# Kernel optimization log

Hardware: AMD Instinct MI355X
Metric: run time of the kernel (lower is better)

## Reference

```python
import jax, jax.numpy as jnp
import numpy as np
from jax import lax

BETA = 0.5
IPOT_ITERS = 20


def cosine_cost(x, y):
    # x: [bs, n, D], y: [bs, m, D] -> 1 - cos_sim, [bs, n, m]
    x = x / (jnp.linalg.norm(x, axis=2, keepdims=True) + 1e-12)
    y = y / (jnp.linalg.norm(y, axis=2, keepdims=True) + 1e-12)
    return 1.0 - jnp.einsum('bnd,bmd->bnm', x, y)


def ipot_T(C, miu, nu, beta=BETA, iters=IPOT_ITERS):
    bs, n, m = C.shape
    A = jnp.exp(-C / beta)                    # [bs, n, m]
    sigma0 = jnp.ones((bs, m, 1), C.dtype) / m
    T0 = jnp.ones((bs, n, m), C.dtype)

    def step(carry, _):
        T, sigma = carry
        T = A * T
        delta = miu[:, :, None] / (T @ sigma + 1e-6)            # [bs, n, 1]
        sigma = nu[:, :, None] / (jnp.swapaxes(T, 1, 2) @ delta + 1e-6)  # [bs, m, 1]
        T = delta * T * jnp.swapaxes(sigma, 1, 2)
        return (T, sigma), None

    (T, _), _ = lax.scan(step, (T0, sigma0), None, length=iters)
    return lax.stop_gradient(T)  # original code detaches T


def ipot_distance(C):
    bs, n, m = C.shape
    miu = jnp.ones((bs, n), C.dtype) / n
    nu = jnp.ones((bs, m), C.dtype) / m
    T = ipot_T(C, miu, nu)
    return -jnp.sum(T * C, axis=(1, 2))  # note: original (un-exponentiated) C


def setup_inputs() -> dict:
    key = jax.random.key(0)
    k1, k2, k3, k4 = jax.random.split(key, 4)
    bs, n_sp, n_tm, D = 128, 196, 32, 768
    return {
        'spatial1': jax.random.normal(k1, (bs, n_sp, D), dtype=jnp.float32),
        'spatial2': jax.random.normal(k2, (bs, n_sp, D), dtype=jnp.float32),
        'temporal1': jax.random.normal(k3, (bs, n_tm, D), dtype=jnp.float32),
        'temporal2': jax.random.normal(k4, (bs, n_tm, D), dtype=jnp.float32),
    }


def reference(spatial1, spatial2, temporal1, temporal2):
    C_sp = cosine_cost(spatial1, spatial2)
    C_tm = cosine_cost(temporal1, temporal2)
    spatial_loss = ipot_distance(C_sp)
    temporal_loss = ipot_distance(C_tm)
    return spatial_loss.mean() + temporal_loss.mean()
```

## Files before the change

### kernel.cpp

```cpp
#include <hip/hip_runtime.h>
#include <hip/hip_bf16.h>
#include <cstdint>

typedef float f32x4 __attribute__((ext_vector_type(4)));
typedef __bf16 bf16x8 __attribute__((ext_vector_type(8)));

#define BS 128
#define NSP 196
#define NTM 32
#define DDIM 768

__device__ inline ushort4 f4_to_bf4(float4 v)
{
    ushort4 u;
    u.x = __builtin_bit_cast(unsigned short, (__bf16)v.x);
    u.y = __builtin_bit_cast(unsigned short, (__bf16)v.y);
    u.z = __builtin_bit_cast(unsigned short, (__bf16)v.z);
    u.w = __builtin_bit_cast(unsigned short, (__bf16)v.w);
    return u;
}

__device__ inline bf16x8 f4x2_to_bf8(float4 lo, float4 hi)
{
    bf16x8 r;
    r[0] = (__bf16)lo.x; r[1] = (__bf16)lo.y; r[2] = (__bf16)lo.z; r[3] = (__bf16)lo.w;
    r[4] = (__bf16)hi.x; r[5] = (__bf16)hi.y; r[6] = (__bf16)hi.z; r[7] = (__bf16)hi.w;
    return r;
}

__device__ inline float sumsq4(float4 a)
{
    return fmaf(a.x, a.x, fmaf(a.y, a.y, fmaf(a.z, a.z, a.w * a.w)));
}

__global__ __launch_bounds__(256)
void tm_norm_kernel(const float* __restrict__ tm1, const float* __restrict__ tm2,
                    float* __restrict__ inx_tm, float* __restrict__ iny_tm)
{
    int B = blockIdx.x;
    const float* src; float* inv;
    if (B < 1024) { src = tm1; inv = inx_tm; }
    else          { B -= 1024; src = tm2; inv = iny_tm; }
    const int row  = B * 4 + (threadIdx.x >> 6);
    const int lane = threadIdx.x & 63;
    const float4* p = reinterpret_cast<const float4*>(src + (size_t)row * DDIM);
    float ss = 0.f;
#pragma unroll
    for (int c = 0; c < 3; ++c) ss += sumsq4(p[lane + 64 * c]);
#pragma unroll
    for (int off = 32; off; off >>= 1) ss += __shfl_xor(ss, off, 64);
    if (lane == 0) inv[row] = 1.0f / (sqrtf(ss) + 1e-12f);
}

#define GA_LDS 18432
__global__ __launch_bounds__(448)
void cost_gemm_spf(const float* __restrict__ X, const float* __restrict__ Y,
                   __bf16* __restrict__ Aout)
{
    __shared__ __bf16 lds[2 * GA_LDS];
    float* ldsF = reinterpret_cast<float*>(lds);

    const int flat  = blockIdx.x;
    const int xcd   = flat & 7;
    const int s     = flat >> 3;
    const int b     = xcd * 16 + (s >> 2);
    const int ctile = s & 3;
    const int n0    = (ctile < 3) ? ctile * 64 : 132;

    const int tid  = threadIdx.x;
    const int w    = tid >> 6, lane = tid & 63;
    const int q    = lane >> 4, l16 = lane & 15;
    const int srow = tid >> 3;
    const int sslt = tid & 7;

    const float* Yb = Y + (size_t)b * NSP * DDIM;

    float4 aL[4], aH[4], bL, bH, b2L, b2H;
    float ssA[4] = {0.f, 0.f, 0.f, 0.f};
    float ssB = 0.f, ssB2 = 0.f;

    auto LOADS = [&](int k0) {
#pragma unroll
        for (int p = 0; p < 4; ++p) {
            int gr = b * NSP + srow + 56 * p;
            gr = min(gr, BS * NSP - 1);
            const float* sp = X + (size_t)gr * DDIM + k0 + sslt * 8;
            aL[p] = *reinterpret_cast<const float4*>(sp);
            aH[p] = *reinterpret_cast<const float4*>(sp + 4);
        }
        {
            const float* sp = Yb + (size_t)(n0 + srow) * DDIM + k0 + sslt * 8;
            bL = *reinterpret_cast<const float4*>(sp);
            bH = *reinterpret_cast<const float4*>(sp + 4);
        }
        if (tid < 64) {
            const float* sp = Yb + (size_t)(n0 + 56 + srow) * DDIM + k0 + sslt * 8;
            b2L = *reinterpret_cast<const float4*>(sp);
            b2H = *reinterpret_cast<const float4*>(sp + 4);
        }
    };
    auto WRITES = [&](int buf) {
#pragma unroll
        for (int p = 0; p < 4; ++p) {
            int r = srow + 56 * p;
            ssA[p] += sumsq4(aL[p]) + sumsq4(aH[p]);
            *reinterpret_cast<bf16x8*>(&lds[buf * GA_LDS + r * 64 + ((sslt ^ (r & 7)) << 3)]) =
                f4x2_to_bf8(aL[p], aH[p]);
        }
        {
            int r = srow;
            ssB += sumsq4(bL) + sumsq4(bH);
            *reinterpret_cast<bf16x8*>(&lds[buf * GA_LDS + 14336 + r * 64 + ((sslt ^ (r & 7)) << 3)]) =
                f4x2_to_bf8(bL, bH);
        }
        if (tid < 64) {
            int r = 56 + srow;
            ssB2 += sumsq4(b2L) + sumsq4(b2H);
            *reinterpret_cast<bf16x8*>(&lds[buf * GA_LDS + 14336 + r * 64 + ((sslt ^ (r & 7)) << 3)]) =
                f4x2_to_bf8(b2L, b2H);
        }
    };

    f32x4 acc[2][4];
#pragma unroll
    for (int i = 0; i < 2; ++i)
#pragma unroll
        for (int j = 0; j < 4; ++j) acc[i][j] = f32x4{0.f, 0.f, 0.f, 0.f};

    LOADS(0);
    int buf = 0;
    for (int kt = 0; kt < 12; ++kt) {
        WRITES(buf);
        if (kt < 11) LOADS((kt + 1) * 64);
        __syncthreads();
#pragma unroll
        for (int ks = 0; ks < 2; ++ks) {
            bf16x8 af[2], bf[4];
#pragma unroll
            for (int rt = 0; rt < 2; ++rt) {
                int r = w * 32 + rt * 16 + l16;
                af[rt] = *reinterpret_cast<const bf16x8*>(
                    &lds[buf * GA_LDS + r * 64 + (((ks * 4 + q) ^ (r & 7)) << 3)]);
            }
#pragma unroll
            for (int ct = 0; ct < 4; ++ct) {
                int r = ct * 16 + l16;
                bf[ct] = *reinterpret_cast<const bf16x8*>(
                    &lds[buf * GA_LDS + 14336 + r * 64 + (((ks * 4 + q) ^ (r & 7)) << 3)]);
            }
#pragma unroll
            for (int ct = 0; ct < 4; ++ct)
#pragma unroll
                for (int rt = 0; rt < 2; ++rt)
                    acc[rt][ct] = __builtin_amdgcn_mfma_f32_16x16x32_bf16(af[rt], bf[ct], acc[rt][ct], 0, 0, 0);
        }
        __syncthreads();
        buf ^= 1;
    }

#pragma unroll
    for (int p = 0; p < 4; ++p) ldsF[(srow + 56 * p) * 8 + sslt] = ssA[p];
    ldsF[1792 + srow * 8 + sslt] = ssB;
    if (tid < 64) ldsF[1792 + (56 + srow) * 8 + sslt] = ssB2;
    __syncthreads();

    float ivy[4];
#pragma unroll
    for (int ct = 0; ct < 4; ++ct) {
        int jr = ct * 16 + l16;
        f32x4 s0 = *reinterpret_cast<const f32x4*>(&ldsF[1792 + jr * 8]);
        f32x4 s1 = *reinterpret_cast<const f32x4*>(&ldsF[1792 + jr * 8 + 4]);
        float ss = (s0.x + s0.y) + (s0.z + s0.w) + (s1.x + s1.y) + (s1.z + s1.w);
        ivy[ct] = 1.0f / (sqrtf(ss) + 1e-12f);
    }
#pragma unroll
    for (int rt = 0; rt < 2; ++rt)
#pragma unroll
        for (int rr = 0; rr < 4; ++rr) {
            int i = w * 32 + rt * 16 + q * 4 + rr;
            if (i < NSP) {
                f32x4 s0 = *reinterpret_cast<const f32x4*>(&ldsF[i * 8]);
                f32x4 s1 = *reinterpret_cast<const f32x4*>(&ldsF[i * 8 + 4]);
                float ss = (s0.x + s0.y) + (s0.z + s0.w) + (s1.x + s1.y) + (s1.z + s1.w);
                float ivx = 1.0f / (sqrtf(ss) + 1e-12f);
#pragma unroll
                for (int ct = 0; ct < 4; ++ct) {
                    float cs = acc[rt][ct][rr] * ivx * ivy[ct];
                    Aout[(size_t)b * 65536 + (size_t)i * 256 + (n0 + ct * 16 + l16)] =
                        (__bf16)__expf(2.0f * cs - 2.0f);
                }
            }
        }
}

template<int WROWS, int NWAVES, int BN, int NPTS>
__global__ __launch_bounds__(NWAVES * 64)
void cost_gemm(const float* __restrict__ X, const float* __restrict__ Y,
               const float* __restrict__ invx, const float* __restrict__ invy,
               float* __restrict__ Aout)
{
    constexpr int MT = WROWS * NWAVES;
    constexpr int CT = BN / 16;
    constexpr int RT = WROWS / 16;
    constexpr int KP = 40;
    constexpr int NTH = NWAVES * 64;
    __shared__ __bf16 As[MT][KP];
    __shared__ __bf16 Bs[BN][KP];

    const int b    = blockIdx.y;
    const int row0 = blockIdx.x * MT;
    const int tid  = threadIdx.x;
    const int w    = tid >> 6, lane = tid & 63;
    const int q    = lane >> 4, l16 = lane & 15;
    const float* Xb = X + (size_t)b * NPTS * DDIM;
    const float* Yb = Y + (size_t)b * NPTS * DDIM;

    f32x4 acc[RT][CT];
#pragma unroll
    for (int i = 0; i < RT; ++i)
#pragma unroll
        for (int j = 0; j < CT; ++j) acc[i][j] = f32x4{0.f, 0.f, 0.f, 0.f};

    for (int k0 = 0; k0 < DDIM; k0 += 32) {
        __syncthreads();
        for (int idx = tid * 4; idx < MT * 32; idx += NTH * 4) {
            int r = idx >> 5, kk = idx & 31;
            int gr = row0 + r;
            float4 v = {0.f, 0.f, 0.f, 0.f};
            if (gr < NPTS) v = *reinterpret_cast<const float4*>(Xb + (size_t)gr * DDIM + k0 + kk);
            *reinterpret_cast<ushort4*>(&As[r][kk]) = f4_to_bf4(v);
        }
        for (int idx = tid * 4; idx < BN * 32; idx += NTH * 4) {
            int r = idx >> 5, kk = idx & 31;
            float4 v = {0.f, 0.f, 0.f, 0.f};
            if (r < NPTS) v = *reinterpret_cast<const float4*>(Yb + (size_t)r * DDIM + k0 + kk);
            *reinterpret_cast<ushort4*>(&Bs[r][kk]) = f4_to_bf4(v);
        }
        __syncthreads();

        bf16x8 af[RT];
#pragma unroll
        for (int rt = 0; rt < RT; ++rt)
            af[rt] = *reinterpret_cast<const bf16x8*>(&As[w * WROWS + rt * 16 + l16][q * 8]);
#pragma unroll
        for (int ct = 0; ct < CT; ++ct) {
            bf16x8 bfr = *reinterpret_cast<const bf16x8*>(&Bs[ct * 16 + l16][q * 8]);
#pragma unroll
            for (int rt = 0; rt < RT; ++rt)
                acc[rt][ct] = __builtin_amdgcn_mfma_f32_16x16x32_bf16(af[rt], bfr, acc[rt][ct], 0, 0, 0);
        }
    }

#pragma unroll
    for (int rt = 0; rt < RT; ++rt)
#pragma unroll
        for (int ct = 0; ct < CT; ++ct)
#pragma unroll
            for (int rr = 0; rr < 4; ++rr) {
                int i = row0 + w * WROWS + rt * 16 + q * 4 + rr;
                int j = ct * 16 + l16;
                if (i < NPTS && j < NPTS) {
                    float g  = acc[rt][ct][rr];
                    float cs = g * invx[b * NPTS + i] * invy[b * NPTS + j];
                    Aout[(size_t)b * NPTS * NPTS + (size_t)i * NPTS + j] = expf(-2.0f * (1.0f - cs));
                }
            }
}

__global__ __launch_bounds__(512, 1)
void ipot_lds(const __bf16* __restrict__ Asp, const float* __restrict__ Atm,
              float* __restrict__ out)
{
    __shared__ __bf16 Alds[224 * 256];
    __shared__ float  cpart[8 * 260];
    __shared__ float  svec[2][272];
    __shared__ float  wsum[8];

    const int B = blockIdx.x;
    if (B >= 128) {
        if (threadIdx.x >= 64) return;
        const int b = B - 128;
        const float* Ab = Atm + (size_t)b * NTM * NTM;
        const int lane = threadIdx.x;
        const int rh = lane >> 5, cj = lane & 31;
        constexpr float MIU = 1.f / NTM;
        float A[16], P[16];
#pragma unroll
        for (int k = 0; k < 16; ++k) {
            A[k] = Ab[(rh + 2 * k) * NTM + cj];
            P[k] = 1.f;
        }
        float sv = MIU;
        for (int it = 0; it < 20; ++it) {
#pragma unroll
            for (int k = 0; k < 16; ++k) {
                P[k] *= A[k];
                float acc = P[k] * sv;
                acc += __shfl_xor(acc, 1);
                acc += __shfl_xor(acc, 2);
                acc += __shfl_xor(acc, 4);
                acc += __shfl_xor(acc, 8);
                acc += __shfl_xor(acc, 16);
                P[k] *= MIU / (acc + 1e-6f);
            }
            float cssum = 0.f;
#pragma unroll
            for (int k = 0; k < 16; ++k) cssum += P[k];
            cssum += __shfl_xor(cssum, 32);
            float sg = MIU / (cssum + 1e-6f);
#pragma unroll
            for (int k = 0; k < 16; ++k) P[k] *= sg;
            sv = sg;
        }
        float acc = 0.f;
#pragma unroll
        for (int k = 0; k < 16; ++k)
            acc = fmaf(P[k], -0.5f * __logf(A[k]), acc);
#pragma unroll
        for (int off = 32; off; off >>= 1) acc += __shfl_xor(acc, off);
        if (lane == 0) atomicAdd(out, -acc * (1.f / BS));
        return;
    }

    const int b = (B & 7) * 16 + (B >> 3);
    const __bf16* Ab = Asp + (size_t)b * 65536;
    const int tid = threadIdx.x;
    const int w = tid >> 6, lane = tid & 63;
    const int rq = lane >> 4, cl = lane & 15;
    const int g = w * 4 + rq;
    const int colbase = cl * 8;
    constexpr float MIU = 1.f / NSP;

    for (int idx = tid; idx < NSP * 32; idx += 512) {
        int r = idx >> 5, c = idx & 31;
        bf16x8 v;
#pragma unroll
        for (int i = 0; i < 8; ++i) v[i] = (__bf16)0.f;
        if (c < 25) {
            v = *reinterpret_cast<const bf16x8*>(&Ab[(size_t)r * 256 + c * 8]);
            if (c == 24) { v[4] = (__bf16)0.f; v[5] = (__bf16)0.f; v[6] = (__bf16)0.f; v[7] = (__bf16)0.f; }
        }
        *reinterpret_cast<bf16x8*>(&Alds[r * 256 + c * 8]) = v;
    }
    {
        ushort4 z = {0, 0, 0, 0};
        for (int idx = tid; idx < 28 * 64; idx += 512) {
            int r = 196 + (idx >> 6), c4 = (idx & 63) << 2;
            *reinterpret_cast<ushort4*>(&Alds[r * 256 + c4]) = z;
        }
    }
    __syncthreads();

    float P[7][16];
#pragma unroll
    for (int k = 0; k < 7; ++k)
#pragma unroll
        for (int e = 0; e < 16; ++e) P[k][e] = 1.f;

    float sr[16];
#pragma unroll
    for (int e = 0; e < 16; ++e) {
        int j = (e < 8) ? (colbase + e) : (colbase + 128 + (e - 8));
        sr[e] = (j < NSP) ? MIU : 0.f;
    }

    for (int it = 0; it < 20; ++it) {
        float cs[16];
#pragma unroll
        for (int e = 0; e < 16; ++e) cs[e] = 0.f;

#pragma unroll
        for (int k = 0; k < 7; ++k) {
            const __bf16* ap = &Alds[(g + 32 * k) * 256 + colbase];
            bf16x8 a0 = *reinterpret_cast<const bf16x8*>(ap);
            bf16x8 a1 = *reinterpret_cast<const bf16x8*>(ap + 128);
            float racc = 0.f;
#pragma unroll
            for (int e = 0; e < 8; ++e) {
                P[k][e] *= (float)a0[e];
                racc = fmaf(P[k][e], sr[e], racc);
            }
#pragma unroll
            for (int e = 0; e < 8; ++e) {
                P[k][8 + e] *= (float)a1[e];
                racc = fmaf(P[k][8 + e], sr[8 + e], racc);
            }
            racc += __shfl_xor(racc, 1);
            racc += __shfl_xor(racc, 2);
            racc += __shfl_xor(racc, 4);
            racc += __shfl_xor(racc, 8);
            float delta = MIU / (racc + 1e-6f);
#pragma unroll
            for (int e = 0; e < 16; ++e) {
                P[k][e] *= delta;
                cs[e] += P[k][e];
            }
        }
#pragma unroll
        for (int e = 0; e < 16; ++e) {
            cs[e] += __shfl_xor(cs[e], 16);
            cs[e] += __shfl_xor(cs[e], 32);
        }
        if (rq == 0) {
            float* cp = &cpart[w * 260 + colbase];
            *reinterpret_cast<f32x4*>(cp)     = f32x4{cs[0], cs[1], cs[2], cs[3]};
            *reinterpret_cast<f32x4*>(cp + 4) = f32x4{cs[4], cs[5], cs[6], cs[7]};
            float* cp2 = cp + 128;
            *reinterpret_cast<f32x4*>(cp2)     = f32x4{cs[8], cs[9], cs[10], cs[11]};
            *reinterpret_cast<f32x4*>(cp2 + 4) = f32x4{cs[12], cs[13], cs[14], cs[15]};
        }
        __syncthreads();
        if (tid < 256) {
            float s0 = 0.f, s1 = 0.f;
#pragma unroll
            for (int gg = 0; gg < 8; gg += 2) {
                s0 += cpart[(gg + 0) * 260 + tid];
                s1 += cpart[(gg + 1) * 260 + tid];
            }
            float sum = s0 + s1;
            svec[it & 1][tid] = (tid < NSP) ? (MIU / (sum + 1e-6f)) : 0.f;
        }
        __syncthreads();
        {
            const float* sv = svec[it & 1];
            f32x4 t0 = *reinterpret_cast<const f32x4*>(&sv[colbase]);
            f32x4 t1 = *reinterpret_cast<const f32x4*>(&sv[colbase + 4]);
            f32x4 t2 = *reinterpret_cast<const f32x4*>(&sv[colbase + 128]);
            f32x4 t3 = *reinterpret_cast<const f32x4*>(&sv[colbase + 132]);
            sr[0] = t0.x; sr[1] = t0.y; sr[2] = t0.z; sr[3] = t0.w;
            sr[4] = t1.x; sr[5] = t1.y; sr[6] = t1.z; sr[7] = t1.w;
            sr[8] = t2.x; sr[9] = t2.y; sr[10] = t2.z; sr[11] = t2.w;
            sr[12] = t3.x; sr[13] = t3.y; sr[14] = t3.z; sr[15] = t3.w;
        }
#pragma unroll
        for (int k = 0; k < 7; ++k)
#pragma unroll
            for (int e = 0; e < 16; ++e) P[k][e] *= sr[e];
    }

    float acc = 0.f;
#pragma unroll
    for (int k = 0; k < 7; ++k) {
        const __bf16* ap = &Alds[(g + 32 * k) * 256 + colbase];
        bf16x8 a0 = *reinterpret_cast<const bf16x8*>(ap);
        bf16x8 a1 = *reinterpret_cast<const bf16x8*>(ap + 128);
#pragma unroll
        for (int e = 0; e < 8; ++e) {
            acc = fmaf(P[k][e],     -0.5f * __logf(fmaxf((float)a0[e], 1e-30f)), acc);
            acc = fmaf(P[k][8 + e], -0.5f * __logf(fmaxf((float)a1[e], 1e-30f)), acc);
        }
    }
#pragma unroll
    for (int off = 32; off; off >>= 1) acc += __shfl_xor(acc, off);
    if (lane == 0) wsum[w] = acc;
    __syncthreads();
    if (tid == 0) {
        float t = 0.f;
#pragma unroll
        for (int i = 0; i < 8; ++i) t += wsum[i];
        atomicAdd(out, -t * (1.f / BS));
    }
}

extern "C" void kernel_launch(void* const* d_in, const int* in_sizes, int n_in,
                              void* d_out, int out_size, void* d_ws, size_t ws_size,
                              hipStream_t stream)
{
    const float* sp1 = (const float*)d_in[0];
    const float* sp2 = (const float*)d_in[1];
    const float* tm1 = (const float*)d_in[2];
    const float* tm2 = (const float*)d_in[3];
    float* out = (float*)d_out;
    float* ws  = (float*)d_ws;

    float* inx_tm = ws;
    float* iny_tm = inx_tm + BS * NTM;
    float* A_tm   = iny_tm + BS * NTM;
    __bf16* A_sp  = (__bf16*)(ws + 139264);

    tm_norm_kernel<<<dim3(2048), 256, 0, stream>>>(tm1, tm2, inx_tm, iny_tm);

    cost_gemm_spf<<<dim3(512), 448, 0, stream>>>(sp1, sp2, A_sp);

    cost_gemm<16, 2, 32, NTM><<<dim3(1, BS), 128, 0, stream>>>(tm1, tm2, inx_tm, iny_tm, A_tm);

    (void)hipMemsetAsync(d_out, 0, sizeof(float), stream);

    ipot_lds<<<dim3(256), 512, 0, stream>>>(A_sp, A_tm, out);
}
```

Measured before the change: 177.6 us.

## Double IPOT block to 1024 threads and pad LDS row stride

The spatial IPOT kernel now runs 16 waves per batch instead of 8. Each thread holds 3-4 row groups of the transport plan instead of 7, and the column partial sums are reduced across 16 waves. The LDS row stride is padded from 256 to 264 to cut bank conflicts on row reads. The aim is more latency hiding and less per-thread serial work in the 20-iteration loop, at the cost of more register pressure per block, two barriers that now span more waves, and extra LDS use.

```diff
diff --git a/kernel.cpp b/kernel.cpp
--- a/kernel.cpp
+++ b/kernel.cpp
@@ -267,14 +267,15 @@
             }
 }
 
-__global__ __launch_bounds__(512, 1)
-void ipot_lds(const __bf16* __restrict__ Asp, const float* __restrict__ Atm,
-              float* __restrict__ out)
-{
-    __shared__ __bf16 Alds[224 * 256];
-    __shared__ float  cpart[8 * 260];
+#define ASTR 264
+__global__ __launch_bounds__(1024, 1)
+void ipot_all2(const __bf16* __restrict__ Asp, const float* __restrict__ Atm,
+               float* __restrict__ out)
+{
+    __shared__ __bf16 Alds[224 * ASTR];
+    __shared__ float  cpart[16 * 260];
     __shared__ float  svec[2][272];
-    __shared__ float  wsum[8];
+    __shared__ float  wsum[16];
 
     const int B = blockIdx.x;
     if (B >= 128) {
@@ -329,9 +330,10 @@
     const int rq = lane >> 4, cl = lane & 15;
     const int g = w * 4 + rq;
     const int colbase = cl * 8;
+    const bool w8 = (w < 8);
     constexpr float MIU = 1.f / NSP;
 
-    for (int idx = tid; idx < NSP * 32; idx += 512) {
+    for (int idx = tid; idx < NSP * 32; idx += 1024) {
         int r = idx >> 5, c = idx & 31;
         bf16x8 v;
 #pragma unroll
@@ -340,20 +342,22 @@
             v = *reinterpret_cast<const bf16x8*>(&Ab[(size_t)r * 256 + c * 8]);
             if (c == 24) { v[4] = (__bf16)0.f; v[5] = (__bf16)0.f; v[6] = (__bf16)0.f; v[7] = (__bf16)0.f; }
         }
-        *reinterpret_cast<bf16x8*>(&Alds[r * 256 + c * 8]) = v;
+        *reinterpret_cast<bf16x8*>(&Alds[r * ASTR + c * 8]) = v;
     }
     {
-        ushort4 z = {0, 0, 0, 0};
-        for (int idx = tid; idx < 28 * 64; idx += 512) {
-            int r = 196 + (idx >> 6), c4 = (idx & 63) << 2;
-            *reinterpret_cast<ushort4*>(&Alds[r * 256 + c4]) = z;
+        bf16x8 z;
+#pragma unroll
+        for (int i = 0; i < 8; ++i) z[i] = (__bf16)0.f;
+        for (int idx = tid; idx < 28 * 32; idx += 1024) {
+            int r = 196 + (idx >> 5), c = idx & 31;
+            *reinterpret_cast<bf16x8*>(&Alds[r * ASTR + c * 8]) = z;
         }
     }
     __syncthreads();
 
-    float P[7][16];
-#pragma unroll
-    for (int k = 0; k < 7; ++k)
+    float P[4][16];
+#pragma unroll
+    for (int k = 0; k < 4; ++k)
 #pragma unroll
         for (int e = 0; e < 16; ++e) P[k][e] = 1.f;
 
@@ -370,8 +374,8 @@
         for (int e = 0; e < 16; ++e) cs[e] = 0.f;
 
 #pragma unroll
-        for (int k = 0; k < 7; ++k) {
-            const __bf16* ap = &Alds[(g + 32 * k) * 256 + colbase];
+        for (int k = 0; k < 3; ++k) {
+            const __bf16* ap = &Alds[(g + 64 * k) * ASTR + colbase];
             bf16x8 a0 = *reinterpret_cast<const bf16x8*>(ap);
             bf16x8 a1 = *reinterpret_cast<const bf16x8*>(ap + 128);
             float racc = 0.f;
@@ -394,6 +398,32 @@
             for (int e = 0; e < 16; ++e) {
                 P[k][e] *= delta;
                 cs[e] += P[k][e];
+            }
+        }
+        if (w8) {
+            const __bf16* ap = &Alds[(192 + g) * ASTR + colbase];
+            bf16x8 a0 = *reinterpret_cast<const bf16x8*>(ap);
+            bf16x8 a1 = *reinterpret_cast<const bf16x8*>(ap + 128);
+            float racc = 0.f;
+#pragma unroll
+            for (int e = 0; e < 8; ++e) {
+                P[3][e] *= (float)a0[e];
+                racc = fmaf(P[3][e], sr[e], racc);
+            }
+#pragma unroll
+            for (int e = 0; e < 8; ++e) {
+                P[3][8 + e] *= (float)a1[e];
+                racc = fmaf(P[3][8 + e], sr[8 + e], racc);
+            }
+            racc += __shfl_xor(racc, 1);
+            racc += __shfl_xor(racc, 2);
+            racc += __shfl_xor(racc, 4);
+            racc += __shfl_xor(racc, 8);
+            float delta = MIU / (racc + 1e-6f);
+#pragma unroll
+            for (int e = 0; e < 16; ++e) {
+                P[3][e] *= delta;
+                cs[e] += P[3][e];
             }
         }
 #pragma unroll
@@ -411,13 +441,15 @@
         }
         __syncthreads();
         if (tid < 256) {
-            float s0 = 0.f, s1 = 0.f;
-#pragma unroll
-            for (int gg = 0; gg < 8; gg += 2) {
+            float s0 = 0.f, s1 = 0.f, s2 = 0.f, s3 = 0.f;
+#pragma unroll
+            for (int gg = 0; gg < 16; gg += 4) {
                 s0 += cpart[(gg + 0) * 260 + tid];
                 s1 += cpart[(gg + 1) * 260 + tid];
-            }
-            float sum = s0 + s1;
+                s2 += cpart[(gg + 2) * 260 + tid];
+                s3 += cpart[(gg + 3) * 260 + tid];
+            }
+            float sum = (s0 + s1) + (s2 + s3);
             svec[it & 1][tid] = (tid < NSP) ? (MIU / (sum + 1e-6f)) : 0.f;
         }
         __syncthreads();
@@ -433,21 +465,31 @@
             sr[12] = t3.x; sr[13] = t3.y; sr[14] = t3.z; sr[15] = t3.w;
         }
 #pragma unroll
-        for (int k = 0; k < 7; ++k)
+        for (int k = 0; k < 4; ++k)
 #pragma unroll
             for (int e = 0; e < 16; ++e) P[k][e] *= sr[e];
     }
 
     float acc = 0.f;
 #pragma unroll
-    for (int k = 0; k < 7; ++k) {
-        const __bf16* ap = &Alds[(g + 32 * k) * 256 + colbase];
+    for (int k = 0; k < 3; ++k) {
+        const __bf16* ap = &Alds[(g + 64 * k) * ASTR + colbase];
         bf16x8 a0 = *reinterpret_cast<const bf16x8*>(ap);
         bf16x8 a1 = *reinterpret_cast<const bf16x8*>(ap + 128);
 #pragma unroll
         for (int e = 0; e < 8; ++e) {
             acc = fmaf(P[k][e],     -0.5f * __logf(fmaxf((float)a0[e], 1e-30f)), acc);
             acc = fmaf(P[k][8 + e], -0.5f * __logf(fmaxf((float)a1[e], 1e-30f)), acc);
+        }
+    }
+    if (w8) {
+        const __bf16* ap = &Alds[(192 + g) * ASTR + colbase];
+        bf16x8 a0 = *reinterpret_cast<const bf16x8*>(ap);
+        bf16x8 a1 = *reinterpret_cast<const bf16x8*>(ap + 128);
+#pragma unroll
+        for (int e = 0; e < 8; ++e) {
+            acc = fmaf(P[3][e],     -0.5f * __logf(fmaxf((float)a0[e], 1e-30f)), acc);
+            acc = fmaf(P[3][8 + e], -0.5f * __logf(fmaxf((float)a1[e], 1e-30f)), acc);
         }
     }
 #pragma unroll
@@ -457,7 +499,7 @@
     if (tid == 0) {
         float t = 0.f;
 #pragma unroll
-        for (int i = 0; i < 8; ++i) t += wsum[i];
+        for (int i = 0; i < 16; ++i) t += wsum[i];
         atomicAdd(out, -t * (1.f / BS));
     }
 }
@@ -486,5 +528,5 @@
 
     (void)hipMemsetAsync(d_out, 0, sizeof(float), stream);
 
-    ipot_lds<<<dim3(256), 512, 0, stream>>>(A_sp, A_tm, out);
-}
+    ipot_all2<<<dim3(256), 1024, 0, stream>>>(A_sp, A_tm, out);
+}
```

Measured after the change: 184.5 us. +3.9%, slower.
